# Optimization experiments

Hardware: AMD Instinct MI355X
Metric: run time of the kernel (lower is better)

Reference implementation:

```python
import jax, jax.numpy as jnp
import numpy as np
from jax import lax

K = 3  # kernel size
KK = K * K


def _bilinear_gather(img, ys, xs):
    """img: [C, H, W]; ys, xs: [KK, H, W] float sample coords.
    Returns [C, KK, H, W], zero outside the image (torch DCN zero-pad semantics)."""
    C, H, W = img.shape
    y0 = jnp.floor(ys).astype(jnp.int32)
    x0 = jnp.floor(xs).astype(jnp.int32)
    y1, x1 = y0 + 1, x0 + 1
    wy1 = ys - y0.astype(ys.dtype)
    wx1 = xs - x0.astype(xs.dtype)
    wy0, wx0 = 1.0 - wy1, 1.0 - wx1

    def g(yi, xi):
        valid = ((yi >= 0) & (yi < H) & (xi >= 0) & (xi < W)).astype(img.dtype)
        yc = jnp.clip(yi, 0, H - 1)
        xc = jnp.clip(xi, 0, W - 1)
        return img[:, yc, xc] * valid[None]  # [C, KK, H, W]

    return (wy0 * wx0) * g(y0, x0) + (wy0 * wx1) * g(y0, x1) \
         + (wy1 * wx0) * g(y1, x0) + (wy1 * wx1) * g(y1, x1)


def _df_layer(x, w_off, b_off, w):
    """One DFConv2d (modulated DCN, k=3, s=1, d=1, pad=1, groups=1) + ReLU."""
    B, C, H, W = x.shape
    O = w.shape[0]
    # offset/mask conv (standard 3x3, pad 1, with bias)
    om = lax.conv_general_dilated(x, w_off, (1, 1), [(1, 1), (1, 1)],
                                  dimension_numbers=('NCHW', 'OIHW', 'NCHW'))
    om = om + b_off[None, :, None, None]                     # [B, 27, H, W]
    off = om[:, :2 * KK].reshape(B, KK, 2, H, W)             # (dy, dx) per kernel pt
    mask = jax.nn.sigmoid(om[:, 2 * KK:3 * KK])              # [B, KK, H, W]

    ki, kj = jnp.meshgrid(jnp.arange(K), jnp.arange(K), indexing='ij')
    # base sampling grid: y = h - pad + i*dil = h + i - 1
    base_y = jnp.arange(H, dtype=x.dtype)[None, :, None] + (ki.reshape(KK, 1, 1).astype(x.dtype) - 1.0)
    base_x = jnp.arange(W, dtype=x.dtype)[None, None, :] + (kj.reshape(KK, 1, 1).astype(x.dtype) - 1.0)
    ys = base_y + off[:, :, 0]                               # [B, KK, H, W]
    xs = base_x + off[:, :, 1]

    sampled = jax.vmap(_bilinear_gather)(x, ys, xs)          # [B, C, KK, H, W]
    out = jnp.einsum('oik,bikhw->bohw', w.reshape(O, C, KK), sampled * mask[:, None])
    return jax.nn.relu(out)


def setup_inputs() -> dict:
    key = jax.random.key(0)
    ks = jax.random.split(key, 7)
    s = 0.05
    return {
        'x': jax.random.normal(ks[0], (2, 256, 96, 96), dtype=jnp.float32),
        'w_off0': jax.random.normal(ks[1], (27, 256, 3, 3), dtype=jnp.float32) * s,
        'b_off0': jnp.zeros((27,), dtype=jnp.float32),
        'w0': jax.random.normal(ks[2], (256, 256, 3, 3), dtype=jnp.float32) * s,
        'w_off1': jax.random.normal(ks[3], (27, 256, 3, 3), dtype=jnp.float32) * s,
        'b_off1': jnp.zeros((27,), dtype=jnp.float32),
        'w1': jax.random.normal(ks[4], (256, 256, 3, 3), dtype=jnp.float32) * s,
    }


def reference(x, w_off0, b_off0, w0, w_off1, b_off1, w1):
    h = _df_layer(x, w_off0, b_off0, w0)
    h = _df_layer(h, w_off1, b_off1, w1)
    return h
```

## Files before the change

kernel.cpp:

```cpp
#include <hip/hip_runtime.h>
#include <cstdint>
#include <cstddef>


#define KTOT 2304
#define PXB  9216

typedef __attribute__((ext_vector_type(8))) short bf16x8;
typedef __attribute__((ext_vector_type(4))) float f32x4;

static __device__ __forceinline__ unsigned short f2bf(float f) {
    union { float f; unsigned int u; } v; v.f = f;
    unsigned int r = (v.u + 0x7FFFu + ((v.u >> 16) & 1u)) >> 16;
    return (unsigned short)r;
}
static __device__ __forceinline__ float bf2f(unsigned short h) {
    union { unsigned int u; float f; } v; v.u = ((unsigned int)h) << 16;
    return v.f;
}
static __device__ __forceinline__ void unpack8(uint4 u, float* f) {
    union { unsigned int u; float f; } t;
    t.u = u.x << 16;         f[0] = t.f;
    t.u = u.x & 0xffff0000u; f[1] = t.f;
    t.u = u.y << 16;         f[2] = t.f;
    t.u = u.y & 0xffff0000u; f[3] = t.f;
    t.u = u.z << 16;         f[4] = t.f;
    t.u = u.z & 0xffff0000u; f[5] = t.f;
    t.u = u.w << 16;         f[6] = t.f;
    t.u = u.w & 0xffff0000u; f[7] = t.f;
}

__global__ __launch_bounds__(256) void transpose_kernel(const float* __restrict__ in,
                                                        unsigned short* __restrict__ outH,
                                                        unsigned short* __restrict__ outL) {
    __shared__ float tile[64][65];
    const int hw0 = blockIdx.x * 64;
    const int c0  = blockIdx.y * 64;
    const int b   = blockIdx.z;
    const int lx  = threadIdx.x & 63;
    const int ly  = threadIdx.x >> 6;
#pragma unroll
    for (int i = 0; i < 16; ++i) {
        int cl = ly + i * 4;
        tile[cl][lx] = in[(size_t)(b * 256 + c0 + cl) * PXB + hw0 + lx];
    }
    __syncthreads();
#pragma unroll
    for (int i = 0; i < 16; ++i) {
        int hwl = ly + i * 4;
        float v = tile[lx][hwl];
        size_t oi = ((size_t)b * PXB + hw0 + hwl) * 256 + c0 + lx;
        unsigned short hi = f2bf(v);
        outH[oi] = hi;
        outL[oi] = f2bf(v - bf2f(hi));
    }
}

__global__ __launch_bounds__(256) void prep_w_kernel(const float* __restrict__ w,
                                                     unsigned short* __restrict__ wA) {
    int idx = blockIdx.x * 256 + threadIdx.x;
    int o = idx / KTOT;
    int k = idx - o * KTOT;
    int kk = k >> 8;
    int c  = k & 255;
    wA[idx] = f2bf(w[o * KTOT + c * 9 + kk]);
}

__global__ __launch_bounds__(256) void prep_woff_kernel(const float* __restrict__ w,
                                                        unsigned short* __restrict__ wH,
                                                        unsigned short* __restrict__ wL) {
    int idx = blockIdx.x * 256 + threadIdx.x;
    int o = idx / KTOT;
    int k = idx - o * KTOT;
    int kk = k >> 8;
    int c  = k & 255;
    float f = (o < 27) ? w[o * KTOT + c * 9 + kk] : 0.0f;
    unsigned short hi = f2bf(f);
    wH[idx] = hi;
    wL[idx] = f2bf(f - bf2f(hi));
}

__global__ __launch_bounds__(512) void offconv_fused(const unsigned short* __restrict__ xH,
                                                     const unsigned short* __restrict__ xL,
                                                     const unsigned short* __restrict__ AH,
                                                     const unsigned short* __restrict__ AL,
                                                     const float* __restrict__ bias,
                                                     float* __restrict__ om) {
    __shared__ __attribute__((aligned(16))) unsigned short AsH[2][32 * 72];
    __shared__ __attribute__((aligned(16))) unsigned short AsL[2][32 * 72];
    __shared__ __attribute__((aligned(16))) unsigned short BsH[2][64 * 72];
    __shared__ __attribute__((aligned(16))) unsigned short BsL[2][64 * 72];

    const int tid  = threadIdx.x;
    const int kg   = tid >> 8;
    const int tl   = tid & 255;
    const int lane = tid & 63;
    const int wq   = (tid >> 6) & 3;
    const int quad = lane >> 4, l16 = lane & 15;
    const int g    = blockIdx.x;
    const int nb   = (g & 7) * 36 + (g >> 3);
    const int n0   = nb * 64;
    const int b    = n0 / PXB;
    const int hw0  = n0 - b * PXB;

    f32x4 acc[2];
#pragma unroll
    for (int mt = 0; mt < 2; ++mt) acc[mt] = (f32x4)0.0f;

    const int arow = tl >> 3, akg = tl & 7;

    uint4 pAH, pAL, pBH0, pBL0, pBH1, pBL1;
    auto pf = [&](int it) {
        const int kt = kg * 18 + it;
        const int kk = kt >> 2, c0 = (kt & 3) * 64;
        const int dy = kk / 3 - 1, dx = kk - (kk / 3) * 3 - 1;
        size_t ai = (size_t)arow * KTOT + kt * 64 + akg * 8;
        pAH = *(const uint4*)&AH[ai];
        pAL = *(const uint4*)&AL[ai];
#pragma unroll
        for (int i = 0; i < 2; ++i) {
            int task = i * 256 + tl;
            int px = task >> 3, cg = task & 7;
            int hw = hw0 + px;
            int h = hw / 96, w = hw - h * 96;
            int y = h + dy, x = w + dx;
            uint4 hv = make_uint4(0u, 0u, 0u, 0u), lv = make_uint4(0u, 0u, 0u, 0u);
            if (((unsigned)y < 96u) && ((unsigned)x < 96u)) {
                size_t bi = ((size_t)b * PXB + y * 96 + x) * 256 + c0 + cg * 8;
                hv = *(const uint4*)&xH[bi];
                lv = *(const uint4*)&xL[bi];
            }
            if (i == 0) { pBH0 = hv; pBL0 = lv; } else { pBH1 = hv; pBL1 = lv; }
        }
    };
    pf(0);

    for (int it = 0; it < 18; ++it) {
        __syncthreads();
        *(uint4*)&AsH[kg][arow * 72 + akg * 8] = pAH;
        *(uint4*)&AsL[kg][arow * 72 + akg * 8] = pAL;
        {
            int px = tl >> 3, cg = tl & 7;
            *(uint4*)&BsH[kg][px * 72 + cg * 8] = pBH0;
            *(uint4*)&BsL[kg][px * 72 + cg * 8] = pBL0;
        }
        {
            int task = 256 + tl;
            int px = task >> 3, cg = task & 7;
            *(uint4*)&BsH[kg][px * 72 + cg * 8] = pBH1;
            *(uint4*)&BsL[kg][px * 72 + cg * 8] = pBL1;
        }
        if (it < 17) pf(it + 1);
        __syncthreads();
#pragma unroll
        for (int ks = 0; ks < 2; ++ks) {
            bf16x8 ah[2], al[2], bh, bl;
#pragma unroll
            for (int mt = 0; mt < 2; ++mt) {
                ah[mt] = *(const bf16x8*)&AsH[kg][(mt * 16 + l16) * 72 + ks * 32 + quad * 8];
                al[mt] = *(const bf16x8*)&AsL[kg][(mt * 16 + l16) * 72 + ks * 32 + quad * 8];
            }
            bh = *(const bf16x8*)&BsH[kg][(wq * 16 + l16) * 72 + ks * 32 + quad * 8];
            bl = *(const bf16x8*)&BsL[kg][(wq * 16 + l16) * 72 + ks * 32 + quad * 8];
#pragma unroll
            for (int mt = 0; mt < 2; ++mt) {
                acc[mt] = __builtin_amdgcn_mfma_f32_16x16x32_bf16(ah[mt], bh, acc[mt], 0, 0, 0);
                acc[mt] = __builtin_amdgcn_mfma_f32_16x16x32_bf16(ah[mt], bl, acc[mt], 0, 0, 0);
                acc[mt] = __builtin_amdgcn_mfma_f32_16x16x32_bf16(al[mt], bh, acc[mt], 0, 0, 0);
            }
        }
    }

    float* red = (float*)BsH;
    __syncthreads();
    if (kg == 1) {
#pragma unroll
        for (int mt = 0; mt < 2; ++mt)
#pragma unroll
            for (int r = 0; r < 4; ++r)
                red[wq * 512 + mt * 256 + quad * 64 + r * 16 + l16] = acc[mt][r];
    }
    __syncthreads();
    if (kg == 0) {
#pragma unroll
        for (int mt = 0; mt < 2; ++mt)
#pragma unroll
            for (int r = 0; r < 4; ++r) {
                float v = acc[mt][r] + red[wq * 512 + mt * 256 + quad * 64 + r * 16 + l16];
                int m = mt * 16 + quad * 4 + r;
                int n = wq * 16 + l16;
                if (m < 27)
                    om[(size_t)(b * 27 + m) * PXB + hw0 + n] = v + bias[m];
            }
    }
}

__global__ __launch_bounds__(512, 4) void dfconv_v4(const unsigned short* __restrict__ xB,
                                                    const float* __restrict__ om,
                                                    const unsigned short* __restrict__ A,
                                                    float* __restrict__ out,
                                                    unsigned short* __restrict__ outH,
                                                    unsigned short* __restrict__ outL,
                                                    int out_mode) {
    __shared__ __attribute__((aligned(16))) char smem[65024];
    unsigned short* BsD  = (unsigned short*)(smem + 32768);
    unsigned short* goff = (unsigned short*)(smem + 51200);
    float*          gwt  = (float*)(smem + 55808);

    const int tid  = threadIdx.x;
    const int wv   = tid >> 6;
    const int lane = tid & 63;
    const int quad = lane >> 4, l16 = lane & 15;
    const int g    = blockIdx.x;
    const int nb   = (g & 7) * 36 + (g >> 3);
    const int n0   = nb * 64;
    const int b    = n0 / PXB;
    const int hw0  = n0 - b * PXB;

    for (int task = tid; task < 576; task += 512) {
        int px = task / 9;
        int kk = task - px * 9;
        int hw = hw0 + px;
        int h = hw / 96, w = hw - h * 96;
        const float* omp = om + (size_t)b * 27 * PXB + hw;
        float dyv = omp[(size_t)(2 * kk) * PXB];
        float dxv = omp[(size_t)(2 * kk + 1) * PXB];
        float mv  = omp[(size_t)(18 + kk) * PXB];
        float mk  = 1.0f / (1.0f + __expf(-mv));

        float ys = (float)(h + (kk / 3) - 1) + dyv;
        float xs = (float)(w + (kk - (kk / 3) * 3) - 1) + dxv;
        float fy = floorf(ys), fx = floorf(xs);
        int iy = (int)fy, ix = (int)fx;
        float wy1 = ys - fy, wx1 = xs - fx;
        float wy0 = 1.0f - wy1, wx0 = 1.0f - wx1;
        bool yv0 = (unsigned)iy < 96u, yv1 = (unsigned)(iy + 1) < 96u;
        bool xv0 = (unsigned)ix < 96u, xv1 = (unsigned)(ix + 1) < 96u;
        int y0 = min(max(iy, 0), 95),     y1 = min(max(iy + 1, 0), 95);
        int x0 = min(max(ix, 0), 95),     x1 = min(max(ix + 1, 0), 95);
        int gg = task * 4;
        goff[gg + 0] = (unsigned short)(y0 * 96 + x0);
        goff[gg + 1] = (unsigned short)(y0 * 96 + x1);
        goff[gg + 2] = (unsigned short)(y1 * 96 + x0);
        goff[gg + 3] = (unsigned short)(y1 * 96 + x1);
        gwt[gg + 0] = (yv0 && xv0) ? mk * wy0 * wx0 : 0.0f;
        gwt[gg + 1] = (yv0 && xv1) ? mk * wy0 * wx1 : 0.0f;
        gwt[gg + 2] = (yv1 && xv0) ? mk * wy1 * wx0 : 0.0f;
        gwt[gg + 3] = (yv1 && xv1) ? mk * wy1 * wx1 : 0.0f;
    }
    __syncthreads();

    const int px = tid >> 3;
    const int cg = tid & 7;
    const unsigned short* xbase = xB + (size_t)b * PXB * 256 + cg * 8;

    const int arl = lane >> 3;
    const int akg = (lane & 7) ^ arl;

    f32x4 acc[2][4];
#pragma unroll
    for (int mt = 0; mt < 2; ++mt)
#pragma unroll
        for (int nt = 0; nt < 4; ++nt) acc[mt][nt] = (f32x4)0.0f;

    auto dmaA = [&](int kt) {
#pragma unroll
        for (int s = 0; s < 4; ++s) {
            const unsigned short* src =
                A + (size_t)(wv * 32 + s * 8 + arl) * KTOT + kt * 64 + akg * 8;
            char* dst = smem + wv * 4096 + s * 1024;
            __builtin_amdgcn_global_load_lds(
                (const __attribute__((address_space(1))) unsigned int*)src,
                (__attribute__((address_space(3))) unsigned int*)dst, 16, 0, 0);
        }
    };

    dmaA(0);
    {
        int gg = (px * 9 + 0) * 4;
        ushort4 o4 = *(const ushort4*)&goff[gg];
        float4 wt = *(const float4*)&gwt[gg];
        uint4 u0 = *(const uint4*)(xbase + (size_t)o4.x * 256);
        uint4 u1 = *(const uint4*)(xbase + (size_t)o4.y * 256);
        uint4 u2 = *(const uint4*)(xbase + (size_t)o4.z * 256);
        uint4 u3 = *(const uint4*)(xbase + (size_t)o4.w * 256);
        float f0[8], f1[8], f2[8], f3[8];
        unpack8(u0, f0); unpack8(u1, f1); unpack8(u2, f2); unpack8(u3, f3);
        unsigned short res[8];
#pragma unroll
        for (int j = 0; j < 8; ++j)
            res[j] = f2bf(wt.x * f0[j] + wt.y * f1[j] + wt.z * f2[j] + wt.w * f3[j]);
        *(uint4*)&BsD[px * 72 + cg * 8] = *(uint4*)res;
    }
    __syncthreads();

    for (int r = 0; r < 36; ++r) {
        const int cur = r & 1;

        uint4 cc0, cc1, cc2, cc3; float4 wt;
        if (r < 35) {
            const int ktn = r + 1, tap = ktn >> 2, c0 = (ktn & 3) * 64;
            int gg = (px * 9 + tap) * 4;
            ushort4 o4 = *(const ushort4*)&goff[gg];
            wt = *(const float4*)&gwt[gg];
            const unsigned short* cb = xbase + c0;
            cc0 = *(const uint4*)(cb + (size_t)o4.x * 256);
            cc1 = *(const uint4*)(cb + (size_t)o4.y * 256);
            cc2 = *(const uint4*)(cb + (size_t)o4.z * 256);
            cc3 = *(const uint4*)(cb + (size_t)o4.w * 256);
        }

        bf16x8 af00, af01, af10, af11;
        {
            const char* Ac = smem + wv * 4096;
            const int sw0 = ((quad ^ (l16 & 7)) * 16);
            const int sw1 = (((4 + quad) ^ (l16 & 7)) * 16);
            af00 = *(const bf16x8*)(Ac + l16 * 128 + sw0);
            af01 = *(const bf16x8*)(Ac + (16 + l16) * 128 + sw0);
            af10 = *(const bf16x8*)(Ac + l16 * 128 + sw1);
            af11 = *(const bf16x8*)(Ac + (16 + l16) * 128 + sw1);
        }
        asm volatile("s_waitcnt lgkmcnt(0)" ::: "memory");
        __builtin_amdgcn_sched_barrier(0);

        if (r < 35) dmaA(r + 1);

        {
            const unsigned short* Br = BsD + cur * 4608;
#pragma unroll
            for (int nt = 0; nt < 4; ++nt) {
                bf16x8 b0 = *(const bf16x8*)&Br[(nt * 16 + l16) * 72 + quad * 8];
                acc[0][nt] = __builtin_amdgcn_mfma_f32_16x16x32_bf16(af00, b0, acc[0][nt], 0, 0, 0);
                acc[1][nt] = __builtin_amdgcn_mfma_f32_16x16x32_bf16(af01, b0, acc[1][nt], 0, 0, 0);
            }
#pragma unroll
            for (int nt = 0; nt < 4; ++nt) {
                bf16x8 b1 = *(const bf16x8*)&Br[(nt * 16 + l16) * 72 + 32 + quad * 8];
                acc[0][nt] = __builtin_amdgcn_mfma_f32_16x16x32_bf16(af10, b1, acc[0][nt], 0, 0, 0);
                acc[1][nt] = __builtin_amdgcn_mfma_f32_16x16x32_bf16(af11, b1, acc[1][nt], 0, 0, 0);
            }
        }

        if (r < 35) {
            unsigned short* Bw = BsD + (cur ^ 1) * 4608;
            float f0[8], f1[8], f2[8], f3[8];
            unpack8(cc0, f0); unpack8(cc1, f1); unpack8(cc2, f2); unpack8(cc3, f3);
            unsigned short res[8];
#pragma unroll
            for (int j = 0; j < 8; ++j)
                res[j] = f2bf(wt.x * f0[j] + wt.y * f1[j] + wt.z * f2[j] + wt.w * f3[j]);
            *(uint4*)&Bw[px * 72 + cg * 8] = *(uint4*)res;
        }

        __syncthreads();
    }

    float* tileS = (float*)smem;
    if (out_mode == 0) {
#pragma unroll
        for (int pass = 0; pass < 4; ++pass) {
            if ((wv >> 1) == pass) {
#pragma unroll
                for (int mt = 0; mt < 2; ++mt)
#pragma unroll
                    for (int nt = 0; nt < 4; ++nt)
#pragma unroll
                        for (int rr = 0; rr < 4; ++rr) {
                            int ml = (wv & 1) * 32 + mt * 16 + quad * 4 + rr;
                            int n  = nt * 16 + l16;
                            tileS[ml * 68 + n] = fmaxf(acc[mt][nt][rr], 0.0f);
                        }
            }
            __syncthreads();
#pragma unroll
            for (int j = 0; j < 2; ++j) {
                int idx = j * 512 + tid;
                int row = idx >> 4, q = idx & 15;
                *(float4*)&out[(size_t)(b * 256 + pass * 64 + row) * PXB + hw0 + q * 4] =
                    *(const float4*)&tileS[row * 68 + q * 4];
            }
            __syncthreads();
        }
    } else {
#pragma unroll
        for (int pass = 0; pass < 4; ++pass) {
#pragma unroll
            for (int mt = 0; mt < 2; ++mt) {
                f32x4 v = acc[mt][pass];
                v[0] = fmaxf(v[0], 0.f); v[1] = fmaxf(v[1], 0.f);
                v[2] = fmaxf(v[2], 0.f); v[3] = fmaxf(v[3], 0.f);
                *(f32x4*)&tileS[l16 * 264 + wv * 32 + mt * 16 + quad * 4] = v;
            }
            __syncthreads();
#pragma unroll
            for (int j = 0; j < 2; ++j) {
                int idx = j * 512 + tid;
                int pxl = idx >> 6, ln = idx & 63;
                float4 v = *(const float4*)&tileS[pxl * 264 + ln * 4];
                size_t oi = ((size_t)b * PXB + hw0 + pass * 16 + pxl) * 256 + ln * 4;
                unsigned short hv[4], lv[4];
#pragma unroll
                for (int e = 0; e < 4; ++e) {
                    float fe = (e == 0) ? v.x : (e == 1) ? v.y : (e == 2) ? v.z : v.w;
                    hv[e] = f2bf(fe);
                    lv[e] = f2bf(fe - bf2f(hv[e]));
                }
                *(ushort4*)&outH[oi] = *(ushort4*)hv;
                *(ushort4*)&outL[oi] = *(ushort4*)lv;
            }
            __syncthreads();
        }
    }
}

extern "C" void kernel_launch(void* const* d_in, const int* in_sizes, int n_in,
                              void* d_out, int out_size, void* d_ws, size_t ws_size,
                              hipStream_t stream) {
    const float* x     = (const float*)d_in[0];
    const float* woff0 = (const float*)d_in[1];
    const float* boff0 = (const float*)d_in[2];
    const float* w0    = (const float*)d_in[3];
    const float* woff1 = (const float*)d_in[4];
    const float* boff1 = (const float*)d_in[5];
    const float* w1    = (const float*)d_in[6];
    float* out = (float*)d_out;

    char* p = (char*)d_ws;
    float* om  = (float*)p;  p += (size_t)2 * 27 * PXB * 4;
    unsigned short* xh  = (unsigned short*)p; p += (size_t)2 * 256 * PXB * 2;
    unsigned short* xl  = (unsigned short*)p; p += (size_t)2 * 256 * PXB * 2;
    unsigned short* h1h = (unsigned short*)p; p += (size_t)2 * 256 * PXB * 2;
    unsigned short* h1l = (unsigned short*)p; p += (size_t)2 * 256 * PXB * 2;
    unsigned short* wA0 = (unsigned short*)p; p += (size_t)256 * KTOT * 2;
    unsigned short* wA1 = (unsigned short*)p; p += (size_t)256 * KTOT * 2;
    unsigned short* wH0 = (unsigned short*)p; p += (size_t)32 * KTOT * 2;
    unsigned short* wL0 = (unsigned short*)p; p += (size_t)32 * KTOT * 2;
    unsigned short* wH1 = (unsigned short*)p; p += (size_t)32 * KTOT * 2;
    unsigned short* wL1 = (unsigned short*)p; p += (size_t)32 * KTOT * 2;

    hipLaunchKernelGGL(transpose_kernel, dim3(PXB / 64, 4, 2), dim3(256), 0, stream, x, xh, xl);
    hipLaunchKernelGGL(prep_w_kernel, dim3(256 * KTOT / 256), dim3(256), 0, stream, w0, wA0);
    hipLaunchKernelGGL(prep_w_kernel, dim3(256 * KTOT / 256), dim3(256), 0, stream, w1, wA1);
    hipLaunchKernelGGL(prep_woff_kernel, dim3(32 * KTOT / 256), dim3(256), 0, stream, woff0, wH0, wL0);
    hipLaunchKernelGGL(prep_woff_kernel, dim3(32 * KTOT / 256), dim3(256), 0, stream, woff1, wH1, wL1);

    hipLaunchKernelGGL(offconv_fused, dim3(288), dim3(512), 0, stream, xh, xl, wH0, wL0, boff0, om);
    hipLaunchKernelGGL(dfconv_v4, dim3(288), dim3(512), 0, stream, xh, om, wA0,
                       (float*)nullptr, h1h, h1l, 1);

    hipLaunchKernelGGL(offconv_fused, dim3(288), dim3(512), 0, stream, h1h, h1l, wH1, wL1, boff1, om);
    hipLaunchKernelGGL(dfconv_v4, dim3(288), dim3(512), 0, stream, h1h, om, wA1,
                       out, (unsigned short*)nullptr, (unsigned short*)nullptr, 0);
}
```

Measured before the change: 316.4 us.

## Retile deformable conv to 72 pixels per block for single-wave 256-block grid

```diff
diff --git a/kernel.cpp b/kernel.cpp
--- a/kernel.cpp
+++ b/kernel.cpp
@@ -195,29 +195,28 @@
     }
 }
 
-__global__ __launch_bounds__(512, 4) void dfconv_v4(const unsigned short* __restrict__ xB,
-                                                    const float* __restrict__ om,
-                                                    const unsigned short* __restrict__ A,
-                                                    float* __restrict__ out,
-                                                    unsigned short* __restrict__ outH,
-                                                    unsigned short* __restrict__ outL,
-                                                    int out_mode) {
-    __shared__ __attribute__((aligned(16))) char smem[65024];
+__global__ __launch_bounds__(512) void dfconv_v5(const unsigned short* __restrict__ xB,
+                                                 const float* __restrict__ om,
+                                                 const unsigned short* __restrict__ A,
+                                                 float* __restrict__ out,
+                                                 unsigned short* __restrict__ outH,
+                                                 unsigned short* __restrict__ outL,
+                                                 int out_mode) {
+    __shared__ __attribute__((aligned(16))) char smem[71360];
     unsigned short* BsD  = (unsigned short*)(smem + 32768);
-    unsigned short* goff = (unsigned short*)(smem + 51200);
-    float*          gwt  = (float*)(smem + 55808);
+    unsigned short* goff = (unsigned short*)(smem + 55808);
+    float*          gwt  = (float*)(smem + 60992);
 
     const int tid  = threadIdx.x;
     const int wv   = tid >> 6;
     const int lane = tid & 63;
     const int quad = lane >> 4, l16 = lane & 15;
     const int g    = blockIdx.x;
-    const int nb   = (g & 7) * 36 + (g >> 3);
-    const int n0   = nb * 64;
-    const int b    = n0 / PXB;
-    const int hw0  = n0 - b * PXB;
-
-    for (int task = tid; task < 576; task += 512) {
+    const int nb   = (g & 7) * 32 + (g >> 3);
+    const int b    = nb >> 7;
+    const int hw0  = (nb & 127) * 72;
+
+    for (int task = tid; task < 648; task += 512) {
         int px = task / 9;
         int kk = task - px * 9;
         int hw = hw0 + px;
@@ -248,20 +247,28 @@
         gwt[gg + 2] = (yv1 && xv0) ? mk * wy1 * wx0 : 0.0f;
         gwt[gg + 3] = (yv1 && xv1) ? mk * wy1 * wx1 : 0.0f;
     }
+    for (int i = tid; i < 576; i += 512) {
+        int buf = i / 288, rem = i - buf * 288;
+        int row = 72 + rem / 36, col2 = (rem - (rem / 36) * 36) * 2;
+        *(unsigned int*)&BsD[buf * 5760 + row * 72 + col2] = 0u;
+    }
     __syncthreads();
 
-    const int px = tid >> 3;
-    const int cg = tid & 7;
-    const unsigned short* xbase = xB + (size_t)b * PXB * 256 + cg * 8;
+    const int px  = tid >> 3;
+    const int cg  = tid & 7;
+    const int px2 = 64 + (tid >> 3);
+    const int cg2 = tid & 7;
+    const unsigned short* xbase  = xB + (size_t)b * PXB * 256 + cg * 8;
+    const unsigned short* xbase2 = xB + (size_t)b * PXB * 256 + cg2 * 8;
 
     const int arl = lane >> 3;
     const int akg = (lane & 7) ^ arl;
 
-    f32x4 acc[2][4];
+    f32x4 acc[2][5];
 #pragma unroll
     for (int mt = 0; mt < 2; ++mt)
 #pragma unroll
-        for (int nt = 0; nt < 4; ++nt) acc[mt][nt] = (f32x4)0.0f;
+        for (int nt = 0; nt < 5; ++nt) acc[mt][nt] = (f32x4)0.0f;
 
     auto dmaA = [&](int kt) {
 #pragma unroll
@@ -292,22 +299,51 @@
             res[j] = f2bf(wt.x * f0[j] + wt.y * f1[j] + wt.z * f2[j] + wt.w * f3[j]);
         *(uint4*)&BsD[px * 72 + cg * 8] = *(uint4*)res;
     }
+    if (tid < 64) {
+        int gg = (px2 * 9 + 0) * 4;
+        ushort4 o4 = *(const ushort4*)&goff[gg];
+        float4 wt = *(const float4*)&gwt[gg];
+        uint4 u0 = *(const uint4*)(xbase2 + (size_t)o4.x * 256);
+        uint4 u1 = *(const uint4*)(xbase2 + (size_t)o4.y * 256);
+        uint4 u2 = *(const uint4*)(xbase2 + (size_t)o4.z * 256);
+        uint4 u3 = *(const uint4*)(xbase2 + (size_t)o4.w * 256);
+        float f0[8], f1[8], f2[8], f3[8];
+        unpack8(u0, f0); unpack8(u1, f1); unpack8(u2, f2); unpack8(u3, f3);
+        unsigned short res[8];
+#pragma unroll
+        for (int j = 0; j < 8; ++j)
+            res[j] = f2bf(wt.x * f0[j] + wt.y * f1[j] + wt.z * f2[j] + wt.w * f3[j]);
+        *(uint4*)&BsD[px2 * 72 + cg2 * 8] = *(uint4*)res;
+    }
     __syncthreads();
 
     for (int r = 0; r < 36; ++r) {
         const int cur = r & 1;
 
         uint4 cc0, cc1, cc2, cc3; float4 wt;
+        uint4 dd0, dd1, dd2, dd3; float4 wt2;
         if (r < 35) {
             const int ktn = r + 1, tap = ktn >> 2, c0 = (ktn & 3) * 64;
-            int gg = (px * 9 + tap) * 4;
-            ushort4 o4 = *(const ushort4*)&goff[gg];
-            wt = *(const float4*)&gwt[gg];
-            const unsigned short* cb = xbase + c0;
-            cc0 = *(const uint4*)(cb + (size_t)o4.x * 256);
-            cc1 = *(const uint4*)(cb + (size_t)o4.y * 256);
-            cc2 = *(const uint4*)(cb + (size_t)o4.z * 256);
-            cc3 = *(const uint4*)(cb + (size_t)o4.w * 256);
+            {
+                int gg = (px * 9 + tap) * 4;
+                ushort4 o4 = *(const ushort4*)&goff[gg];
+                wt = *(const float4*)&gwt[gg];
+                const unsigned short* cb = xbase + c0;
+                cc0 = *(const uint4*)(cb + (size_t)o4.x * 256);
+                cc1 = *(const uint4*)(cb + (size_t)o4.y * 256);
+                cc2 = *(const uint4*)(cb + (size_t)o4.z * 256);
+                cc3 = *(const uint4*)(cb + (size_t)o4.w * 256);
+            }
+            if (tid < 64) {
+                int gg = (px2 * 9 + tap) * 4;
+                ushort4 o4 = *(const ushort4*)&goff[gg];
+                wt2 = *(const float4*)&gwt[gg];
+                const unsigned short* cb = xbase2 + c0;
+                dd0 = *(const uint4*)(cb + (size_t)o4.x * 256);
+                dd1 = *(const uint4*)(cb + (size_t)o4.y * 256);
+                dd2 = *(const uint4*)(cb + (size_t)o4.z * 256);
+                dd3 = *(const uint4*)(cb + (size_t)o4.w * 256);
+            }
         }
 
         bf16x8 af00, af01, af10, af11;
@@ -326,15 +362,15 @@
         if (r < 35) dmaA(r + 1);
 
         {
-            const unsigned short* Br = BsD + cur * 4608;
-#pragma unroll
-            for (int nt = 0; nt < 4; ++nt) {
+            const unsigned short* Br = BsD + cur * 5760;
+#pragma unroll
+            for (int nt = 0; nt < 5; ++nt) {
                 bf16x8 b0 = *(const bf16x8*)&Br[(nt * 16 + l16) * 72 + quad * 8];
                 acc[0][nt] = __builtin_amdgcn_mfma_f32_16x16x32_bf16(af00, b0, acc[0][nt], 0, 0, 0);
                 acc[1][nt] = __builtin_amdgcn_mfma_f32_16x16x32_bf16(af01, b0, acc[1][nt], 0, 0, 0);
             }
 #pragma unroll
-            for (int nt = 0; nt < 4; ++nt) {
+            for (int nt = 0; nt < 5; ++nt) {
                 bf16x8 b1 = *(const bf16x8*)&Br[(nt * 16 + l16) * 72 + 32 + quad * 8];
                 acc[0][nt] = __builtin_amdgcn_mfma_f32_16x16x32_bf16(af10, b1, acc[0][nt], 0, 0, 0);
                 acc[1][nt] = __builtin_amdgcn_mfma_f32_16x16x32_bf16(af11, b1, acc[1][nt], 0, 0, 0);
@@ -342,14 +378,25 @@
         }
 
         if (r < 35) {
-            unsigned short* Bw = BsD + (cur ^ 1) * 4608;
-            float f0[8], f1[8], f2[8], f3[8];
-            unpack8(cc0, f0); unpack8(cc1, f1); unpack8(cc2, f2); unpack8(cc3, f3);
-            unsigned short res[8];
-#pragma unroll
-            for (int j = 0; j < 8; ++j)
-                res[j] = f2bf(wt.x * f0[j] + wt.y * f1[j] + wt.z * f2[j] + wt.w * f3[j]);
-            *(uint4*)&Bw[px * 72 + cg * 8] = *(uint4*)res;
+            unsigned short* Bw = BsD + (cur ^ 1) * 5760;
+            {
+                float f0[8], f1[8], f2[8], f3[8];
+                unpack8(cc0, f0); unpack8(cc1, f1); unpack8(cc2, f2); unpack8(cc3, f3);
+                unsigned short res[8];
+#pragma unroll
+                for (int j = 0; j < 8; ++j)
+                    res[j] = f2bf(wt.x * f0[j] + wt.y * f1[j] + wt.z * f2[j] + wt.w * f3[j]);
+                *(uint4*)&Bw[px * 72 + cg * 8] = *(uint4*)res;
+            }
+            if (tid < 64) {
+                float f0[8], f1[8], f2[8], f3[8];
+                unpack8(dd0, f0); unpack8(dd1, f1); unpack8(dd2, f2); unpack8(dd3, f3);
+                unsigned short res[8];
+#pragma unroll
+                for (int j = 0; j < 8; ++j)
+                    res[j] = f2bf(wt2.x * f0[j] + wt2.y * f1[j] + wt2.z * f2[j] + wt2.w * f3[j]);
+                *(uint4*)&Bw[px2 * 72 + cg2 * 8] = *(uint4*)res;
+            }
         }
 
         __syncthreads();
@@ -363,27 +410,29 @@
 #pragma unroll
                 for (int mt = 0; mt < 2; ++mt)
 #pragma unroll
-                    for (int nt = 0; nt < 4; ++nt)
+                    for (int nt = 0; nt < 5; ++nt)
 #pragma unroll
                         for (int rr = 0; rr < 4; ++rr) {
                             int ml = (wv & 1) * 32 + mt * 16 + quad * 4 + rr;
                             int n  = nt * 16 + l16;
-                            tileS[ml * 68 + n] = fmaxf(acc[mt][nt][rr], 0.0f);
+                            tileS[ml * 80 + n] = fmaxf(acc[mt][nt][rr], 0.0f);
                         }
             }
             __syncthreads();
 #pragma unroll
-            for (int j = 0; j < 2; ++j) {
+            for (int j = 0; j < 3; ++j) {
                 int idx = j * 512 + tid;
-                int row = idx >> 4, q = idx & 15;
-                *(float4*)&out[(size_t)(b * 256 + pass * 64 + row) * PXB + hw0 + q * 4] =
-                    *(const float4*)&tileS[row * 68 + q * 4];
+                if (idx < 1152) {
+                    int row = idx / 18, q = idx - row * 18;
+                    *(float4*)&out[(size_t)(b * 256 + pass * 64 + row) * PXB + hw0 + q * 4] =
+                        *(const float4*)&tileS[row * 80 + q * 4];
+                }
             }
             __syncthreads();
         }
     } else {
 #pragma unroll
-        for (int pass = 0; pass < 4; ++pass) {
+        for (int pass = 0; pass < 5; ++pass) {
 #pragma unroll
             for (int mt = 0; mt < 2; ++mt) {
                 f32x4 v = acc[mt][pass];
@@ -392,21 +441,24 @@
                 *(f32x4*)&tileS[l16 * 264 + wv * 32 + mt * 16 + quad * 4] = v;
             }
             __syncthreads();
+            const int cnt = (pass < 4) ? 1024 : 512;
 #pragma unroll
             for (int j = 0; j < 2; ++j) {
                 int idx = j * 512 + tid;
-                int pxl = idx >> 6, ln = idx & 63;
-                float4 v = *(const float4*)&tileS[pxl * 264 + ln * 4];
-                size_t oi = ((size_t)b * PXB + hw0 + pass * 16 + pxl) * 256 + ln * 4;
-                unsigned short hv[4], lv[4];
-#pragma unroll
-                for (int e = 0; e < 4; ++e) {
-                    float fe = (e == 0) ? v.x : (e == 1) ? v.y : (e == 2) ? v.z : v.w;
-                    hv[e] = f2bf(fe);
-                    lv[e] = f2bf(fe - bf2f(hv[e]));
+                if (idx < cnt) {
+                    int pxl = idx >> 6, ln = idx & 63;
+                    float4 v = *(const float4*)&tileS[pxl * 264 + ln * 4];
+                    size_t oi = ((size_t)b * PXB + hw0 + pass * 16 + pxl) * 256 + ln * 4;
+                    unsigned short hv[4], lv[4];
+#pragma unroll
+                    for (int e = 0; e < 4; ++e) {
+                        float fe = (e == 0) ? v.x : (e == 1) ? v.y : (e == 2) ? v.z : v.w;
+                        hv[e] = f2bf(fe);
+                        lv[e] = f2bf(fe - bf2f(hv[e]));
+                    }
+                    *(ushort4*)&outH[oi] = *(ushort4*)hv;
+                    *(ushort4*)&outL[oi] = *(ushort4*)lv;
                 }
-                *(ushort4*)&outH[oi] = *(ushort4*)hv;
-                *(ushort4*)&outL[oi] = *(ushort4*)lv;
             }
             __syncthreads();
         }
@@ -445,10 +497,10 @@
     hipLaunchKernelGGL(prep_woff_kernel, dim3(32 * KTOT / 256), dim3(256), 0, stream, woff1, wH1, wL1);
 
     hipLaunchKernelGGL(offconv_fused, dim3(288), dim3(512), 0, stream, xh, xl, wH0, wL0, boff0, om);
-    hipLaunchKernelGGL(dfconv_v4, dim3(288), dim3(512), 0, stream, xh, om, wA0,
+    hipLaunchKernelGGL(dfconv_v5, dim3(256), dim3(512), 0, stream, xh, om, wA0,
                        (float*)nullptr, h1h, h1l, 1);
 
     hipLaunchKernelGGL(offconv_fused, dim3(288), dim3(512), 0, stream, h1h, h1l, wH1, wL1, boff1, om);
-    hipLaunchKernelGGL(dfconv_v4, dim3(288), dim3(512), 0, stream, h1h, om, wA1,
+    hipLaunchKernelGGL(dfconv_v5, dim3(256), dim3(512), 0, stream, h1h, om, wA1,
                        out, (unsigned short*)nullptr, (unsigned short*)nullptr, 0);
 }
```

New measurement: 274.6 us. 1.15x faster.
